# Optimization experiments

Measured on AMD Instinct MI355X. Metric: run time of the kernel, lower is better.

Reference implementation:

```python
import jax, jax.numpy as jnp
import numpy as np

N = 131072
D = 512        # input_dim
H = 512        # hidden_dim
E = 10         # num_experts
INIT_STD_SCALE = 0.1


def _trunc_normal(key, shape, std):
    # approximate trunc_normal_(std=std) in [-2std, 2std]
    return jnp.clip(jax.random.normal(key, shape) * std, -2.0 * std, 2.0 * std).astype(jnp.float32)


def setup_inputs() -> dict:
    key = jax.random.key(0)
    ks = jax.random.split(key, 6)
    x = jax.random.normal(ks[0], (N, D), dtype=jnp.float32)
    # router (default nn.Linear init approximated with uniform)
    lim = 1.0 / np.sqrt(D)
    Wr = jax.random.uniform(ks[1], (E, D), minval=-lim, maxval=lim, dtype=jnp.float32)
    br = jnp.zeros((E,), dtype=jnp.float32)
    # experts: trunc_normal with std = 0.1 / sqrt(fan_in), zero bias
    W1 = _trunc_normal(ks[2], (E, D, H), INIT_STD_SCALE / np.sqrt(D))   # [E, D, H]
    b1 = jnp.zeros((E, H), dtype=jnp.float32)
    W2 = _trunc_normal(ks[3], (E, H, H), INIT_STD_SCALE / np.sqrt(H))   # [E, H, H]
    b2 = jnp.zeros((E, H), dtype=jnp.float32)
    return {"x": x, "Wr": Wr, "br": br, "W1": W1, "b1": b1, "W2": W2, "b2": b2}


def reference(x, Wr, br, W1, b1, W2, b2):
    # router in fp32 (autocast disabled in original)
    logits = x.astype(jnp.float32) @ Wr.T + br          # [N, E]
    expert_ids = jnp.argmax(logits, axis=1)              # [N]
    out = jnp.zeros((x.shape[0], W2.shape[-1]), dtype=x.dtype)
    # fixed small loop over experts; dropout is identity at inference
    for e in range(W1.shape[0]):
        h = jax.nn.relu(x @ W1[e] + b1[e])                # [N, H]
        o = h @ W2[e] + b2[e]                             # [N, H]
        out = jnp.where((expert_ids == e)[:, None], o, out)
    return out, expert_ids
```

## Files before the change

kernel.cpp:

```cpp
#include <hip/hip_runtime.h>
#include <hip/hip_bf16.h>

#define N_TOK 131072
#define DIM   512
#define HID   512
#define NEXP  10

using bf16x8 = __attribute__((ext_vector_type(8))) short;
using f32x4  = __attribute__((ext_vector_type(4))) float;

__device__ __forceinline__ short f2bf(float f) {
    union { float f; unsigned u; } v; v.f = f;
    unsigned u = v.u;
    return (short)((u + 0x7FFFu + ((u >> 16) & 1u)) >> 16);
}

#define GLOAD16(g, l) __builtin_amdgcn_global_load_lds( \
    (const __attribute__((address_space(1))) void*)(g),  \
    (__attribute__((address_space(3))) void*)(l), 16, 0, 0)

__global__ __launch_bounds__(256) void router_kernel(
    const float* __restrict__ x, const float* __restrict__ Wr,
    const float* __restrict__ br, int* __restrict__ eid,
    float* __restrict__ ids_out, int* __restrict__ counts,
    short* __restrict__ xb)
{
    __shared__ float wr[NEXP][DIM];
    __shared__ int lcnt[NEXP];
    int tid = threadIdx.x;
    for (int i = tid; i < NEXP * DIM / 4; i += 256)
        ((float4*)wr)[i] = ((const float4*)Wr)[i];
    if (tid < NEXP) lcnt[tid] = 0;
    __syncthreads();

    int lane  = tid & 63;
    int wave  = tid >> 6;
    int gwave = blockIdx.x * 4 + wave;
    int nwav  = gridDim.x * 4;

    for (int t = gwave; t < N_TOK; t += nwav) {
        const float4* xr = (const float4*)(x + (size_t)t * DIM);
        float4 v0 = xr[lane * 2], v1 = xr[lane * 2 + 1];
        float xf[8] = {v0.x, v0.y, v0.z, v0.w, v1.x, v1.y, v1.z, v1.w};
        bf16x8 p;
        #pragma unroll
        for (int j = 0; j < 8; ++j) p[j] = f2bf(xf[j]);
        *(bf16x8*)(xb + (size_t)t * DIM + lane * 8) = p;

        float dot[NEXP];
        #pragma unroll
        for (int e = 0; e < NEXP; ++e) {
            const float* wv = &wr[e][lane * 8];
            float s = 0.f;
            #pragma unroll
            for (int j = 0; j < 8; ++j) s = fmaf(xf[j], wv[j], s);
            dot[e] = s;
        }
        #pragma unroll
        for (int off = 32; off > 0; off >>= 1) {
            #pragma unroll
            for (int e = 0; e < NEXP; ++e) dot[e] += __shfl_xor(dot[e], off, 64);
        }
        if (lane == 0) {
            int best = 0; float bv = dot[0] + br[0];
            #pragma unroll
            for (int e = 1; e < NEXP; ++e) {
                float v = dot[e] + br[e];
                if (v > bv) { bv = v; best = e; }
            }
            eid[t] = best;
            ids_out[t] = (float)best;
            atomicAdd(&lcnt[best], 1);
        }
    }
    __syncthreads();
    if (tid < NEXP) atomicAdd(&counts[tid], lcnt[tid]);
}

__global__ void offsets_kernel(const int* __restrict__ counts,
                               int* __restrict__ offsets, int* __restrict__ toff)
{
    if (threadIdx.x == 0) {
        int acc = 0, ta = 0;
        for (int e = 0; e < NEXP; ++e) {
            offsets[e] = acc; toff[e] = ta;
            acc += counts[e]; ta += (counts[e] + 127) >> 7;
        }
        offsets[NEXP] = acc; toff[NEXP] = ta;
    }
}

__global__ __launch_bounds__(256) void scatter_kernel(
    const int* __restrict__ eid, const int* __restrict__ offsets,
    int* __restrict__ cursors, int* __restrict__ perm)
{
    __shared__ int lcnt[NEXP], lbase[NEXP];
    int tid = threadIdx.x;
    if (tid < NEXP) lcnt[tid] = 0;
    __syncthreads();
    int t = blockIdx.x * 256 + tid;
    int e = 0, lpos = 0;
    if (t < N_TOK) {
        e = eid[t];
        lpos = atomicAdd(&lcnt[e], 1);
    }
    __syncthreads();
    if (tid < NEXP) lbase[tid] = atomicAdd(&cursors[tid], lcnt[tid]);
    __syncthreads();
    if (t < N_TOK) perm[offsets[e] + lbase[e] + lpos] = t;
}

__global__ __launch_bounds__(256) void wconvert_kernel(
    const float* __restrict__ W1, const float* __restrict__ W2,
    short* __restrict__ W1b, short* __restrict__ W2b)
{
    int mat = blockIdx.z;
    const float* src = (mat < NEXP) ? W1 + (size_t)mat * 512 * 512
                                    : W2 + (size_t)(mat - NEXP) * 512 * 512;
    short* dst = (mat < NEXP) ? W1b + (size_t)mat * 512 * 512
                              : W2b + (size_t)(mat - NEXP) * 512 * 512;
    __shared__ float tile[64][65];
    int r0 = blockIdx.y * 64, c0 = blockIdx.x * 64;
    int tid = threadIdx.x;
    int tr = tid >> 4, tc4 = (tid & 15) * 4;
    #pragma unroll
    for (int i = 0; i < 4; ++i) {
        float4 v = *(const float4*)(src + (size_t)(r0 + i * 16 + tr) * 512 + c0 + tc4);
        tile[i * 16 + tr][tc4 + 0] = v.x; tile[i * 16 + tr][tc4 + 1] = v.y;
        tile[i * 16 + tr][tc4 + 2] = v.z; tile[i * 16 + tr][tc4 + 3] = v.w;
    }
    __syncthreads();
    int s   = (r0 + tc4) >> 5;
    int kin = (r0 + tc4) & 31;
    #pragma unroll
    for (int i = 0; i < 4; ++i) {
        int cc = i * 16 + tr;
        ushort4 o;
        o.x = (ushort)f2bf(tile[tc4 + 0][cc]); o.y = (ushort)f2bf(tile[tc4 + 1][cc]);
        o.z = (ushort)f2bf(tile[tc4 + 2][cc]); o.w = (ushort)f2bf(tile[tc4 + 3][cc]);
        *(ushort4*)(dst + (size_t)s * 16384 + (size_t)(c0 + cc) * 32 + kin) = o;
    }
}

template<int LAYER>
__global__ __launch_bounds__(512, 4) void expert_gemm(
    const short* __restrict__ xb, const short* __restrict__ hA,
    const short* __restrict__ WT, const float* __restrict__ bias,
    const int* __restrict__ offsets, const int* __restrict__ toff,
    const int* __restrict__ perm,
    short* __restrict__ hOut, float* __restrict__ out)
{
    int g = blockIdx.x;
    if (g >= toff[NEXP]) return;
    int e = 0;
    #pragma unroll
    for (int k = 1; k < NEXP; ++k) e += (g >= toff[k]);
    int beg = offsets[e], cnt = offsets[e + 1] - beg;
    int m0 = (g - toff[e]) * 128;
    int nb = blockIdx.y * 256;

    __shared__ int toks[128];
    __shared__ short Ab[3][128 * 32];
    __shared__ short Bb[3][256 * 32];

    int tid = threadIdx.x, lane = tid & 63, w = tid >> 6;
    if (tid < 128) toks[tid] = perm[beg + min(m0 + tid, cnt - 1)];
    __syncthreads();

    int srow = w * 16 + (lane >> 2);
    int slot = lane & 3;
    const short* WTe  = WT + (size_t)e * 512 * 512;
    const short* bSrc = WTe + (size_t)(nb + srow) * 32 + slot * 8;
    const short* aSrc;
    if (LAYER == 1) aSrc = xb + (size_t)toks[srow] * DIM + slot * 8;
    else            aSrc = hA + (size_t)(beg + min(m0 + srow, cnt - 1)) * HID + slot * 8;

    auto stage = [&](int t, int b) {
        GLOAD16(bSrc + t * 16384,        (char*)&Bb[b][0] + w * 1024);
        GLOAD16(bSrc + t * 16384 + 4096, (char*)&Bb[b][0] + 8192 + w * 1024);
        GLOAD16(aSrc + t * 32,           (char*)&Ab[b][0] + w * 1024);
    };

    f32x4 acc[4][4];
    #pragma unroll
    for (int i = 0; i < 4; ++i)
        #pragma unroll
        for (int j = 0; j < 4; ++j) acc[i][j] = (f32x4){0.f, 0.f, 0.f, 0.f};

    int wr = w >> 2, wc = w & 3;
    int lrow = lane & 15;
    int lk   = (lane >> 4) * 8;

    auto comp = [&](int b) {
        const short* A = &Ab[b][0];
        const short* B = &Bb[b][0];
        bf16x8 af[4], bv[4];
        #pragma unroll
        for (int i = 0; i < 4; ++i)
            af[i] = *(const bf16x8*)(A + (wr * 64 + i * 16 + lrow) * 32 + lk);
        #pragma unroll
        for (int j = 0; j < 4; ++j)
            bv[j] = *(const bf16x8*)(B + (wc * 64 + j * 16 + lrow) * 32 + lk);
        __builtin_amdgcn_s_setprio(1);
        #pragma unroll
        for (int i = 0; i < 4; ++i)
            #pragma unroll
            for (int j = 0; j < 4; ++j)
                acc[i][j] = __builtin_amdgcn_mfma_f32_16x16x32_bf16(af[i], bv[j], acc[i][j], 0, 0, 0);
        __builtin_amdgcn_s_setprio(0);
    };

    stage(0, 0);
    stage(1, 1);
    asm volatile("s_waitcnt vmcnt(3)" ::: "memory");
    __builtin_amdgcn_s_barrier();

    #pragma unroll
    for (int t = 0; t < 16; ++t) {
        if (t + 2 < 16) stage(t + 2, (t + 2) % 3);
        comp(t % 3);
        if (t == 15) break;
        if (t + 2 < 16) asm volatile("s_waitcnt vmcnt(3)" ::: "memory");
        else            asm volatile("s_waitcnt vmcnt(0)" ::: "memory");
        __builtin_amdgcn_s_barrier();
    }

    const float* be = bias + (size_t)e * 512;
    int colb = nb + wc * 64 + lrow;
    float bv[4];
    #pragma unroll
    for (int j = 0; j < 4; ++j) bv[j] = be[colb + j * 16];

    #pragma unroll
    for (int i = 0; i < 4; ++i) {
        #pragma unroll
        for (int q = 0; q < 4; ++q) {
            int rr = wr * 64 + i * 16 + ((lane >> 4) << 2) + q;
            if (m0 + rr < cnt) {
                if (LAYER == 1) {
                    short* hp = hOut + (size_t)(beg + m0 + rr) * HID + colb;
                    #pragma unroll
                    for (int j = 0; j < 4; ++j) {
                        float v = acc[i][j][q] + bv[j];
                        hp[j * 16] = f2bf(v > 0.f ? v : 0.f);
                    }
                } else {
                    float* op = out + (size_t)toks[rr] * HID + colb;
                    #pragma unroll
                    for (int j = 0; j < 4; ++j)
                        op[j * 16] = acc[i][j][q] + bv[j];
                }
            }
        }
    }
}

extern "C" void kernel_launch(void* const* d_in, const int* in_sizes, int n_in,
                              void* d_out, int out_size, void* d_ws, size_t ws_size,
                              hipStream_t stream)
{
    const float* x  = (const float*)d_in[0];
    const float* Wr = (const float*)d_in[1];
    const float* br = (const float*)d_in[2];
    const float* W1 = (const float*)d_in[3];
    const float* b1 = (const float*)d_in[4];
    const float* W2 = (const float*)d_in[5];
    const float* b2 = (const float*)d_in[6];

    float* out     = (float*)d_out;
    float* ids_out = out + (size_t)N_TOK * HID;

    char* ws     = (char*)d_ws;
    int* counts  = (int*)ws;
    int* offsets = counts + 16;
    int* toff    = counts + 32;
    int* cursors = counts + 48;
    int* eid     = (int*)(ws + 1024);
    int* perm    = eid + N_TOK;
    short* W1b   = (short*)(ws + 1024 + (size_t)2 * N_TOK * 4);
    short* W2b   = W1b + (size_t)NEXP * 512 * 512;
    short* h     = W2b + (size_t)NEXP * 512 * 512;
    short* xb    = h   + (size_t)N_TOK * HID;

    hipMemsetAsync(d_ws, 0, 1024, stream);
    router_kernel<<<2048, 256, 0, stream>>>(x, Wr, br, eid, ids_out, counts, xb);
    wconvert_kernel<<<dim3(8, 8, 2 * NEXP), 256, 0, stream>>>(W1, W2, W1b, W2b);
    offsets_kernel<<<1, 64, 0, stream>>>(counts, offsets, toff);
    scatter_kernel<<<512, 256, 0, stream>>>(eid, offsets, cursors, perm);

    int ntiles = (N_TOK + 127) / 128 + NEXP;
    expert_gemm<1><<<dim3(ntiles, 2), 512, 0, stream>>>(xb, nullptr, W1b, b1, offsets, toff, perm, h, nullptr);
    expert_gemm<2><<<dim3(ntiles, 2), 512, 0, stream>>>(nullptr, h, W2b, b2, offsets, toff, perm, nullptr, out);
}
```

Baseline: 367.0 us.

## Enlarge expert GEMM tile to 256x256 with K=64 double-buffered, swizzled LDS

Each expert-GEMM block now covers 256 tokens instead of 128, with 8x4 accumulator fragments per wave. The K loop steps by 64 using two 64KB LDS buffers, and the next tile's loads are issued in four chunks interleaved with the MFMA phases. LDS rows are XOR-swizzled to cut bank conflicts, and the offsets kernel and grid are resized to match. The goal is more arithmetic per byte loaded and fewer barriers per FLOP, at the cost of higher register and LDS use. That lowers occupancy to about one to two blocks per CU and wastes more padding on partial expert tiles.

```diff
diff --git a/kernel.cpp b/kernel.cpp
--- a/kernel.cpp
+++ b/kernel.cpp
@@ -84,7 +84,7 @@
         int acc = 0, ta = 0;
         for (int e = 0; e < NEXP; ++e) {
             offsets[e] = acc; toff[e] = ta;
-            acc += counts[e]; ta += (counts[e] + 127) >> 7;
+            acc += counts[e]; ta += (counts[e] + 255) >> 8;
         }
         offsets[NEXP] = acc; toff[NEXP] = ta;
     }
@@ -143,7 +143,7 @@
 }
 
 template<int LAYER>
-__global__ __launch_bounds__(512, 4) void expert_gemm(
+__global__ __launch_bounds__(512, 2) void expert_gemm(
     const short* __restrict__ xb, const short* __restrict__ hA,
     const short* __restrict__ WT, const float* __restrict__ bias,
     const int* __restrict__ offsets, const int* __restrict__ toff,
@@ -156,99 +156,127 @@
     #pragma unroll
     for (int k = 1; k < NEXP; ++k) e += (g >= toff[k]);
     int beg = offsets[e], cnt = offsets[e + 1] - beg;
-    int m0 = (g - toff[e]) * 128;
+    int m0 = (g - toff[e]) * 256;
     int nb = blockIdx.y * 256;
 
-    __shared__ int toks[128];
-    __shared__ short Ab[3][128 * 32];
-    __shared__ short Bb[3][256 * 32];
+    __shared__ int toks[256];
+    __shared__ short lds_s[65536];
 
     int tid = threadIdx.x, lane = tid & 63, w = tid >> 6;
-    if (tid < 128) toks[tid] = perm[beg + min(m0 + tid, cnt - 1)];
-    __syncthreads();
-
-    int srow = w * 16 + (lane >> 2);
-    int slot = lane & 3;
-    const short* WTe  = WT + (size_t)e * 512 * 512;
-    const short* bSrc = WTe + (size_t)(nb + srow) * 32 + slot * 8;
-    const short* aSrc;
-    if (LAYER == 1) aSrc = xb + (size_t)toks[srow] * DIM + slot * 8;
-    else            aSrc = hA + (size_t)(beg + min(m0 + srow, cnt - 1)) * HID + slot * 8;
-
-    auto stage = [&](int t, int b) {
-        GLOAD16(bSrc + t * 16384,        (char*)&Bb[b][0] + w * 1024);
-        GLOAD16(bSrc + t * 16384 + 4096, (char*)&Bb[b][0] + 8192 + w * 1024);
-        GLOAD16(aSrc + t * 32,           (char*)&Ab[b][0] + w * 1024);
+    if (tid < 256) toks[tid] = perm[beg + min(m0 + tid, cnt - 1)];
+    __syncthreads();
+
+    char* LDS = (char*)lds_s;
+    const short* WTe = WT + (size_t)e * 512 * 512;
+
+    const short* aBase[2];
+    const short* bBase[2];
+    int ldsOff[2];
+    #pragma unroll
+    for (int k = 0; k < 2; ++k) {
+        int s   = w * 128 + k * 64 + lane;
+        int row = s >> 2;
+        int ql  = (s & 3) ^ (row & 3);
+        bBase[k] = WTe + (size_t)(nb + row) * 32 + ql * 8;
+        if (LAYER == 1) aBase[k] = xb + (size_t)toks[row] * DIM + ql * 8;
+        else            aBase[k] = hA + (size_t)(beg + min(m0 + row, cnt - 1)) * HID + ql * 8;
+        ldsOff[k] = w * 2048 + k * 1024;
+    }
+
+    auto stage_chunk = [&](int ti, int c, int b) {
+        int kh  = c >> 1;
+        if (c & 1) {
+            char* dst = LDS + b * 65536 + kh * 16384;
+            GLOAD16(aBase[0] + ti * 64 + kh * 32, dst + ldsOff[0]);
+            GLOAD16(aBase[1] + ti * 64 + kh * 32, dst + ldsOff[1]);
+        } else {
+            char* dst = LDS + b * 65536 + 32768 + kh * 16384;
+            GLOAD16(bBase[0] + (ti * 2 + kh) * 16384, dst + ldsOff[0]);
+            GLOAD16(bBase[1] + (ti * 2 + kh) * 16384, dst + ldsOff[1]);
+        }
     };
 
-    f32x4 acc[4][4];
-    #pragma unroll
-    for (int i = 0; i < 4; ++i)
+    int wr = w >> 2, wc = w & 3, lrow = lane & 15;
+    int qp = (lane >> 4) ^ (lane & 3);
+    int offA0 = (wr * 128 + lrow) * 64 + qp * 16;
+    int offB0 = 32768 + (wc * 64 + lrow) * 64 + qp * 16;
+
+    f32x4 acc[8][4];
+    #pragma unroll
+    for (int i = 0; i < 8; ++i)
         #pragma unroll
         for (int j = 0; j < 4; ++j) acc[i][j] = (f32x4){0.f, 0.f, 0.f, 0.f};
 
-    int wr = w >> 2, wc = w & 3;
-    int lrow = lane & 15;
-    int lk   = (lane >> 4) * 8;
-
-    auto comp = [&](int b) {
-        const short* A = &Ab[b][0];
-        const short* B = &Bb[b][0];
-        bf16x8 af[4], bv[4];
-        #pragma unroll
-        for (int i = 0; i < 4; ++i)
-            af[i] = *(const bf16x8*)(A + (wr * 64 + i * 16 + lrow) * 32 + lk);
-        #pragma unroll
-        for (int j = 0; j < 4; ++j)
-            bv[j] = *(const bf16x8*)(B + (wc * 64 + j * 16 + lrow) * 32 + lk);
-        __builtin_amdgcn_s_setprio(1);
-        #pragma unroll
-        for (int i = 0; i < 4; ++i)
-            #pragma unroll
-            for (int j = 0; j < 4; ++j)
-                acc[i][j] = __builtin_amdgcn_mfma_f32_16x16x32_bf16(af[i], bv[j], acc[i][j], 0, 0, 0);
-        __builtin_amdgcn_s_setprio(0);
-    };
-
-    stage(0, 0);
-    stage(1, 1);
-    asm volatile("s_waitcnt vmcnt(3)" ::: "memory");
-    __builtin_amdgcn_s_barrier();
-
-    #pragma unroll
-    for (int t = 0; t < 16; ++t) {
-        if (t + 2 < 16) stage(t + 2, (t + 2) % 3);
-        comp(t % 3);
-        if (t == 15) break;
-        if (t + 2 < 16) asm volatile("s_waitcnt vmcnt(3)" ::: "memory");
-        else            asm volatile("s_waitcnt vmcnt(0)" ::: "memory");
-        __builtin_amdgcn_s_barrier();
+    stage_chunk(0, 0, 0); stage_chunk(0, 1, 0);
+    stage_chunk(0, 2, 0); stage_chunk(0, 3, 0);
+
+    bf16x8 bv[4];
+
+    #pragma unroll
+    for (int i = 0; i < 8; ++i) {
+        int b = i & 1;
+        char* cbuf = LDS + b * 65536;
+        #pragma unroll
+        for (int p = 0; p < 4; ++p) {
+            int kh = p >> 1, rh = p & 1;
+            if (p == 0) {
+                asm volatile("s_waitcnt vmcnt(4)" ::: "memory");
+            } else if (p == 2) {
+                if (i == 7) asm volatile("s_waitcnt vmcnt(0)" ::: "memory");
+                else        asm volatile("s_waitcnt vmcnt(4)" ::: "memory");
+            }
+            __builtin_amdgcn_s_barrier();
+            __builtin_amdgcn_sched_barrier(0);
+
+            if (rh == 0) {
+                #pragma unroll
+                for (int cf = 0; cf < 4; ++cf)
+                    bv[cf] = *(const bf16x8*)(cbuf + offB0 + cf * 1024 + kh * 16384);
+            }
+            bf16x8 af[4];
+            #pragma unroll
+            for (int r = 0; r < 4; ++r) {
+                int i8 = rh * 4 + r;
+                af[r] = *(const bf16x8*)(cbuf + offA0 + i8 * 1024 + kh * 16384);
+            }
+
+            if (i < 7) stage_chunk(i + 1, p, b ^ 1);
+
+            __builtin_amdgcn_s_setprio(1);
+            #pragma unroll
+            for (int r = 0; r < 4; ++r)
+                #pragma unroll
+                for (int cf = 0; cf < 4; ++cf)
+                    acc[rh * 4 + r][cf] =
+                        __builtin_amdgcn_mfma_f32_16x16x32_bf16(af[r], bv[cf], acc[rh * 4 + r][cf], 0, 0, 0);
+            __builtin_amdgcn_s_setprio(0);
+        }
     }
 
     const float* be = bias + (size_t)e * 512;
     int colb = nb + wc * 64 + lrow;
-    float bv[4];
-    #pragma unroll
-    for (int j = 0; j < 4; ++j) bv[j] = be[colb + j * 16];
-
-    #pragma unroll
-    for (int i = 0; i < 4; ++i) {
+    float bvv[4];
+    #pragma unroll
+    for (int j = 0; j < 4; ++j) bvv[j] = be[colb + j * 16];
+
+    #pragma unroll
+    for (int i = 0; i < 8; ++i) {
         #pragma unroll
         for (int q = 0; q < 4; ++q) {
-            int rr = wr * 64 + i * 16 + ((lane >> 4) << 2) + q;
+            int rr = wr * 128 + i * 16 + ((lane >> 4) << 2) + q;
             if (m0 + rr < cnt) {
                 if (LAYER == 1) {
                     short* hp = hOut + (size_t)(beg + m0 + rr) * HID + colb;
                     #pragma unroll
                     for (int j = 0; j < 4; ++j) {
-                        float v = acc[i][j][q] + bv[j];
+                        float v = acc[i][j][q] + bvv[j];
                         hp[j * 16] = f2bf(v > 0.f ? v : 0.f);
                     }
                 } else {
                     float* op = out + (size_t)toks[rr] * HID + colb;
                     #pragma unroll
                     for (int j = 0; j < 4; ++j)
-                        op[j * 16] = acc[i][j][q] + bv[j];
+                        op[j * 16] = acc[i][j][q] + bvv[j];
                 }
             }
         }
@@ -288,7 +316,7 @@
     offsets_kernel<<<1, 64, 0, stream>>>(counts, offsets, toff);
     scatter_kernel<<<512, 256, 0, stream>>>(eid, offsets, cursors, perm);
 
-    int ntiles = (N_TOK + 127) / 128 + NEXP;
+    int ntiles = (N_TOK + 255) / 256 + NEXP;
     expert_gemm<1><<<dim3(ntiles, 2), 512, 0, stream>>>(xb, nullptr, W1b, b1, offsets, toff, perm, h, nullptr);
     expert_gemm<2><<<dim3(ntiles, 2), 512, 0, stream>>>(nullptr, h, W2b, b2, offsets, toff, perm, nullptr, out);
 }
```

Result: slower. 392.5 us (+6.9%).

## Shrink expert GEMM tile to 128x128 with 4 waves and XOR-swizzled LDS

Applied to the files above, without the earlier changes.

The expert GEMM block tile goes from 128x256 with 8 waves to 128x128 with 4 waves, and the grid doubles along N. Staging now issues two A and two B loads per thread, and the vmcnt waits are adjusted to match. An XOR swizzle of the 16-byte k-chunks, keyed on the row index, is applied to both the global_load_lds destinations and the LDS fragment reads, to cut LDS bank conflicts. The smaller tile loads each A row twice as often across the N dimension and lowers per-block reuse, in exchange for more blocks and possibly better occupancy.

```diff
diff --git a/kernel.cpp b/kernel.cpp
--- a/kernel.cpp
+++ b/kernel.cpp
@@ -143,7 +143,7 @@
 }
 
 template<int LAYER>
-__global__ __launch_bounds__(512, 4) void expert_gemm(
+__global__ __launch_bounds__(256, 3) void expert_gemm(
     const short* __restrict__ xb, const short* __restrict__ hA,
     const short* __restrict__ WT, const float* __restrict__ bias,
     const int* __restrict__ offsets, const int* __restrict__ toff,
@@ -157,50 +157,62 @@
     for (int k = 1; k < NEXP; ++k) e += (g >= toff[k]);
     int beg = offsets[e], cnt = offsets[e + 1] - beg;
     int m0 = (g - toff[e]) * 128;
-    int nb = blockIdx.y * 256;
+    int nb = blockIdx.y * 128;
 
     __shared__ int toks[128];
     __shared__ short Ab[3][128 * 32];
-    __shared__ short Bb[3][256 * 32];
+    __shared__ short Bb[3][128 * 32];
 
     int tid = threadIdx.x, lane = tid & 63, w = tid >> 6;
     if (tid < 128) toks[tid] = perm[beg + min(m0 + tid, cnt - 1)];
     __syncthreads();
 
-    int srow = w * 16 + (lane >> 2);
-    int slot = lane & 3;
-    const short* WTe  = WT + (size_t)e * 512 * 512;
-    const short* bSrc = WTe + (size_t)(nb + srow) * 32 + slot * 8;
-    const short* aSrc;
-    if (LAYER == 1) aSrc = xb + (size_t)toks[srow] * DIM + slot * 8;
-    else            aSrc = hA + (size_t)(beg + min(m0 + srow, cnt - 1)) * HID + slot * 8;
+    const short* WTe = WT + (size_t)e * 512 * 512;
+    const short* aSrc[2];
+    const short* bSrc[2];
+    #pragma unroll
+    for (int k = 0; k < 2; ++k) {
+        int s   = w * 128 + k * 64 + lane;
+        int row = s >> 2;
+        int ql  = (s & 3) ^ ((row >> 1) & 3);
+        bSrc[k] = WTe + (size_t)(nb + row) * 32 + ql * 8;
+        if (LAYER == 1) aSrc[k] = xb + (size_t)toks[row] * DIM + ql * 8;
+        else            aSrc[k] = hA + (size_t)(beg + min(m0 + row, cnt - 1)) * HID + ql * 8;
+    }
 
     auto stage = [&](int t, int b) {
-        GLOAD16(bSrc + t * 16384,        (char*)&Bb[b][0] + w * 1024);
-        GLOAD16(bSrc + t * 16384 + 4096, (char*)&Bb[b][0] + 8192 + w * 1024);
-        GLOAD16(aSrc + t * 32,           (char*)&Ab[b][0] + w * 1024);
+        #pragma unroll
+        for (int k = 0; k < 2; ++k) {
+            GLOAD16(aSrc[k] + t * 32,    (char*)&Ab[b][0] + w * 2048 + k * 1024);
+            GLOAD16(bSrc[k] + t * 16384, (char*)&Bb[b][0] + w * 2048 + k * 1024);
+        }
     };
 
+    int wr = w >> 1, wc = w & 1, lrow = lane & 15, kq = lane >> 4;
+    int offA[4], offB[4];
+    #pragma unroll
+    for (int i = 0; i < 4; ++i) {
+        int r = wr * 64 + i * 16 + lrow;
+        offA[i] = r * 64 + (kq ^ ((r >> 1) & 3)) * 16;
+    }
+    #pragma unroll
+    for (int j = 0; j < 4; ++j) {
+        int r = wc * 64 + j * 16 + lrow;
+        offB[j] = r * 64 + (kq ^ ((r >> 1) & 3)) * 16;
+    }
+
     f32x4 acc[4][4];
     #pragma unroll
     for (int i = 0; i < 4; ++i)
         #pragma unroll
         for (int j = 0; j < 4; ++j) acc[i][j] = (f32x4){0.f, 0.f, 0.f, 0.f};
 
-    int wr = w >> 2, wc = w & 3;
-    int lrow = lane & 15;
-    int lk   = (lane >> 4) * 8;
-
     auto comp = [&](int b) {
-        const short* A = &Ab[b][0];
-        const short* B = &Bb[b][0];
         bf16x8 af[4], bv[4];
         #pragma unroll
-        for (int i = 0; i < 4; ++i)
-            af[i] = *(const bf16x8*)(A + (wr * 64 + i * 16 + lrow) * 32 + lk);
-        #pragma unroll
-        for (int j = 0; j < 4; ++j)
-            bv[j] = *(const bf16x8*)(B + (wc * 64 + j * 16 + lrow) * 32 + lk);
+        for (int i = 0; i < 4; ++i) af[i] = *(const bf16x8*)((char*)&Ab[b][0] + offA[i]);
+        #pragma unroll
+        for (int j = 0; j < 4; ++j) bv[j] = *(const bf16x8*)((char*)&Bb[b][0] + offB[j]);
         __builtin_amdgcn_s_setprio(1);
         #pragma unroll
         for (int i = 0; i < 4; ++i)
@@ -212,7 +224,7 @@
 
     stage(0, 0);
     stage(1, 1);
-    asm volatile("s_waitcnt vmcnt(3)" ::: "memory");
+    asm volatile("s_waitcnt vmcnt(4)" ::: "memory");
     __builtin_amdgcn_s_barrier();
 
     #pragma unroll
@@ -220,35 +232,35 @@
         if (t + 2 < 16) stage(t + 2, (t + 2) % 3);
         comp(t % 3);
         if (t == 15) break;
-        if (t + 2 < 16) asm volatile("s_waitcnt vmcnt(3)" ::: "memory");
+        if (t + 2 < 16) asm volatile("s_waitcnt vmcnt(4)" ::: "memory");
         else            asm volatile("s_waitcnt vmcnt(0)" ::: "memory");
         __builtin_amdgcn_s_barrier();
     }
 
     const float* be = bias + (size_t)e * 512;
     int colb = nb + wc * 64 + lrow;
-    float bv[4];
-    #pragma unroll
-    for (int j = 0; j < 4; ++j) bv[j] = be[colb + j * 16];
+    float bvv[4];
+    #pragma unroll
+    for (int j = 0; j < 4; ++j) bvv[j] = be[colb + j * 16];
 
     #pragma unroll
     for (int i = 0; i < 4; ++i) {
         #pragma unroll
         for (int q = 0; q < 4; ++q) {
-            int rr = wr * 64 + i * 16 + ((lane >> 4) << 2) + q;
+            int rr = wr * 64 + i * 16 + kq * 4 + q;
             if (m0 + rr < cnt) {
                 if (LAYER == 1) {
                     short* hp = hOut + (size_t)(beg + m0 + rr) * HID + colb;
                     #pragma unroll
                     for (int j = 0; j < 4; ++j) {
-                        float v = acc[i][j][q] + bv[j];
+                        float v = acc[i][j][q] + bvv[j];
                         hp[j * 16] = f2bf(v > 0.f ? v : 0.f);
                     }
                 } else {
                     float* op = out + (size_t)toks[rr] * HID + colb;
                     #pragma unroll
                     for (int j = 0; j < 4; ++j)
-                        op[j * 16] = acc[i][j][q] + bv[j];
+                        op[j * 16] = acc[i][j][q] + bvv[j];
                 }
             }
         }
@@ -289,6 +301,6 @@
     scatter_kernel<<<512, 256, 0, stream>>>(eid, offsets, cursors, perm);
 
     int ntiles = (N_TOK + 127) / 128 + NEXP;
-    expert_gemm<1><<<dim3(ntiles, 2), 512, 0, stream>>>(xb, nullptr, W1b, b1, offsets, toff, perm, h, nullptr);
-    expert_gemm<2><<<dim3(ntiles, 2), 512, 0, stream>>>(nullptr, h, W2b, b2, offsets, toff, perm, nullptr, out);
-}
+    expert_gemm<1><<<dim3(ntiles, 4), 256, 0, stream>>>(xb, nullptr, W1b, b1, offsets, toff, perm, h, nullptr);
+    expert_gemm<2><<<dim3(ntiles, 4), 256, 0, stream>>>(nullptr, h, W2b, b2, offsets, toff, perm, nullptr, out);
+}
```

Measured after the change: 408.0 us. 11.2% more time.
